# Kernel tuning notes

Measured on AMD Instinct MI355X. Metric: run time of the kernel, lower is better.

The kernel has to match this reference:

```python
import jax, jax.numpy as jnp
import numpy as np

D_MODEL, N_HEADS, D_K, D_V = 512, 8, 32, 32
LN_EPS = 1e-5


def setup_inputs() -> dict:
    key = jax.random.key(0)
    ks = jax.random.split(key, 12)
    B, L = 4, 2048
    inner = N_HEADS * D_K
    s_in = 1.0 / np.sqrt(D_MODEL)
    s_fc = 1.0 / np.sqrt(inner)
    return {
        "q": jax.random.normal(ks[0], (B, L, D_MODEL), jnp.float32),
        "k": jax.random.normal(ks[1], (B, L, D_MODEL), jnp.float32),
        "v": jax.random.normal(ks[2], (B, L, D_MODEL), jnp.float32),
        "Wq": jax.random.normal(ks[3], (inner, D_MODEL), jnp.float32) * s_in,
        "bq": jax.random.normal(ks[4], (inner,), jnp.float32) * 0.01,
        "Wk": jax.random.normal(ks[5], (inner, D_MODEL), jnp.float32) * s_in,
        "bk": jax.random.normal(ks[6], (inner,), jnp.float32) * 0.01,
        "Wv": jax.random.normal(ks[7], (N_HEADS * D_V, D_MODEL), jnp.float32) * s_in,
        "bv": jax.random.normal(ks[8], (N_HEADS * D_V,), jnp.float32) * 0.01,
        "Wfc": jax.random.normal(ks[9], (D_MODEL, N_HEADS * D_V), jnp.float32) * s_fc,
        "bfc": jax.random.normal(ks[10], (D_MODEL,), jnp.float32) * 0.01,
        "gamma": jnp.ones((D_MODEL,), jnp.float32),
        "beta": jnp.zeros((D_MODEL,), jnp.float32),
    }


def reference(q, k, v, Wq, bq, Wk, bk, Wv, bv, Wfc, bfc, gamma, beta):
    n, l, _ = q.shape
    # Projection output interpreted as (..., d_k, n_heads): head idx is fastest dim
    def split_heads(x, W, b, dh):
        p = x @ W.T + b                     # [n, l, dh*H]
        return p.reshape(n, x.shape[1], dh, N_HEADS).transpose(0, 3, 1, 2)  # [n,H,l,dh]

    qh = split_heads(q, Wq, bq, D_K)
    kh = split_heads(k, Wk, bk, D_K)
    vh = split_heads(v, Wv, bv, D_V)

    scale = 1.0 / jnp.sqrt(jnp.asarray(D_K, q.dtype))
    scores = jnp.einsum('nhqd,nhkd->nhqk', qh, kh) * scale  # [n,H,L,L]
    att = jax.nn.softmax(scores, axis=-1)
    out = jnp.einsum('nhqk,nhkd->nhqd', att, vh)             # [n,H,L,d_v]
    out = out.transpose(0, 2, 1, 3).reshape(n, l, N_HEADS * D_V)

    fc = out @ Wfc.T + bfc
    x = fc + q  # residual
    mean = jnp.mean(x, axis=-1, keepdims=True)
    var = jnp.mean(jnp.square(x - mean), axis=-1, keepdims=True)
    return gamma * (x - mean) / jnp.sqrt(var + LN_EPS) + beta
```

## Files before the change

### kernel.cpp

```cpp
#include <hip/hip_runtime.h>
#include <math.h>

constexpr int Bn = 4, Ln = 2048, DM = 512, NH = 8, DKv = 32, INNER = 256;
constexpr int TTOK = Bn * Ln;
constexpr size_t HEAD_ELEMS = (size_t)Bn * NH * Ln * DKv;


typedef short short8 __attribute__((ext_vector_type(8)));
typedef short short4v __attribute__((ext_vector_type(4)));
typedef float floatx4 __attribute__((ext_vector_type(4)));

constexpr size_t XB_OFF  = 8u * 1024 * 1024;
constexpr size_t WB_OFF  = 12536832;
constexpr size_t WFCB_OFF = WB_OFF + 3 * 131072;

constexpr float C1 = 0.25505654f;

__device__ inline short f2bf(float x) {
  unsigned u = __builtin_bit_cast(unsigned, x);
  unsigned r = (u + 0x7FFFu + ((u >> 16) & 1u)) >> 16;
  return (short)r;
}

#if __has_builtin(__builtin_amdgcn_mfma_f32_16x16x16bf16_1k)
#define MFMA16(a, b, c) __builtin_amdgcn_mfma_f32_16x16x16bf16_1k(a, b, c, 0, 0, 0)
#else
__device__ inline floatx4 mfma16_asm(short4v a, short4v b, floatx4 c) {
  asm volatile("v_mfma_f32_16x16x16_bf16 %0, %1, %2, %3\n\ts_nop 4"
               : "=v"(c) : "v"(a), "v"(b), "0"(c));
  return c;
}
#define MFMA16(a, b, c) mfma16_asm(a, b, c)
#endif

__global__ __launch_bounds__(256) void cvtw_kernel(
    const float* __restrict__ Wq, const float* __restrict__ Wk,
    const float* __restrict__ Wv, const float* __restrict__ Wfc,
    short* __restrict__ Wb, short* __restrict__ Wfcb)
{
  const int z = blockIdx.y;
  const float* src = z == 0 ? Wq : (z == 1 ? Wk : (z == 2 ? Wv : Wfc));
  short* dst = z < 3 ? Wb + (size_t)z * 131072 : Wfcb;
  const int idx = (blockIdx.x * 256 + threadIdx.x) * 4;
  float4 x = *(const float4*)&src[idx];
  *(short4v*)&dst[idx] = (short4v){f2bf(x.x), f2bf(x.y), f2bf(x.z), f2bf(x.w)};
}

__global__ __launch_bounds__(256) void proj_kernel(
    const float* __restrict__ q, const float* __restrict__ k, const float* __restrict__ v,
    const short* __restrict__ Wb,
    const float* __restrict__ bq, const float* __restrict__ bk,
    const float* __restrict__ bv,
    short* __restrict__ ws)
{
  const int mat = blockIdx.z;
  const float* X    = mat == 0 ? q  : (mat == 1 ? k  : v);
  const short* W    = Wb + (size_t)mat * 131072;
  const float* bias = mat == 0 ? bq : (mat == 1 ? bk : bv);
  short* outp = ws + (size_t)mat * HEAD_ELEMS;

  const int t0 = blockIdx.x * 64;
  const int c0 = blockIdx.y * 64;
  const int tid = threadIdx.x;
  const int col = tid & 15;
  const int quad = (tid & 63) >> 4;
  const int w = tid >> 6;

  __shared__ short Xs[64 * 136];
  __shared__ short Wsh[64 * 136];

  floatx4 acc[4];
#pragma unroll
  for (int nj = 0; nj < 4; ++nj) acc[nj] = (floatx4){0.f, 0.f, 0.f, 0.f};

  float4 xr[8];
  short8 wr[4];
  auto loadX = [&](int k0) {
#pragma unroll
    for (int j = 0; j < 8; ++j) {
      const int i = tid + j * 256, row = i >> 5, c4 = i & 31;
      xr[j] = *(const float4*)&X[(size_t)(t0 + row) * DM + k0 + c4 * 4];
    }
  };
  auto loadW = [&](int k0) {
#pragma unroll
    for (int j = 0; j < 4; ++j) {
      const int s = tid + j * 256, row = s >> 4, k8 = s & 15;
      wr[j] = *(const short8*)&W[(size_t)(c0 + row) * DM + k0 + k8 * 8];
    }
  };

  loadX(0);
  loadW(0);

  for (int kc = 0; kc < 4; ++kc) {
#pragma unroll
    for (int j = 0; j < 8; ++j) {
      const int i = tid + j * 256, row = i >> 5, c4 = i & 31;
      *(short4v*)&Xs[row * 136 + c4 * 4] =
          (short4v){f2bf(xr[j].x), f2bf(xr[j].y), f2bf(xr[j].z), f2bf(xr[j].w)};
    }
#pragma unroll
    for (int j = 0; j < 4; ++j) {
      const int s = tid + j * 256, row = s >> 4, k8 = s & 15;
      *(short8*)&Wsh[row * 136 + k8 * 8] = wr[j];
    }
    __syncthreads();
    if (kc < 3) {
      loadX((kc + 1) * 128);
      loadW((kc + 1) * 128);
    }
#pragma unroll
    for (int ks = 0; ks < 4; ++ks) {
      short8 a = *(const short8*)&Xs[(w * 16 + col) * 136 + ks * 32 + quad * 8];
#pragma unroll
      for (int nj = 0; nj < 4; ++nj) {
        short8 b = *(const short8*)&Wsh[(nj * 16 + col) * 136 + ks * 32 + quad * 8];
        acc[nj] = __builtin_amdgcn_mfma_f32_16x16x32_bf16(a, b, acc[nj], 0, 0, 0);
      }
    }
    __syncthreads();
  }

#pragma unroll
  for (int nj = 0; nj < 4; ++nj) {
#pragma unroll
    for (int r = 0; r < 4; ++r) {
      const int t = t0 + w * 16 + quad * 4 + r;
      const int n = t >> 11, ll = t & (Ln - 1);
      const int c = c0 + nj * 16 + col;
      const int d = c >> 3, h = c & 7;
      float pv = acc[nj][r] + bias[c];
      if (mat == 0) pv *= C1;
      const short val = f2bf(pv);
      if (mat < 2)
        outp[((size_t)(n * NH + h) * Ln + ll) * DKv + d] = val;
      else
        outp[((size_t)(n * NH + h) * DKv + d) * Ln + ll] = val;
    }
  }
}

__global__ __launch_bounds__(256) void attn_kernel(const short* __restrict__ ws,
                                                   short* __restrict__ O2b)
{
  const int bh = blockIdx.y;
  const int n = bh >> 3, h = bh & 7;
  const int tid = threadIdx.x;
  const int col = tid & 15;
  const int quad = (tid & 63) >> 4;
  const int w = tid >> 6;
  const int qi = blockIdx.x * 64 + w * 16 + col;

  const short* Qh = ws;
  const short* Kg = ws + HEAD_ELEMS + (size_t)bh * Ln * DKv;
  const short* Vg = ws + 2 * HEAD_ELEMS + (size_t)bh * DKv * Ln;

  __shared__ short Ks[2][64 * 32];
  __shared__ short Vs[2][64 * 32];

  const short8 aq = *(const short8*)&Qh[(size_t)bh * Ln * DKv + (size_t)qi * DKv + quad * 8];

  float lsum = 0.f;
  floatx4 o[2];
  o[0] = (floatx4){0.f, 0.f, 0.f, 0.f};
  o[1] = (floatx4){0.f, 0.f, 0.f, 0.f};

  const int vd = tid >> 3, vkb = tid & 7;
  const int voff1 = (vkb >> 1) * 512 + ((2 * vkb) & 3) * 128 + (vd & 15) * 8 + (vd >> 4) * 4;
  const int voff2 = (vkb >> 1) * 512 + ((2 * vkb + 1) & 3) * 128 + (vd & 15) * 8 + (vd >> 4) * 4;

  short8 kr = *(const short8*)(Kg + tid * 8);
  short8 vr = *(const short8*)(Vg + (size_t)vd * Ln + vkb * 8);

  for (int kt = 0; kt < 32; ++kt) {
    short* ksb = Ks[kt & 1];
    short* vsb = Vs[kt & 1];
    *(short8*)&ksb[tid * 8] = kr;
    *(short4v*)&vsb[voff1] = __builtin_shufflevector(vr, vr, 0, 1, 2, 3);
    *(short4v*)&vsb[voff2] = __builtin_shufflevector(vr, vr, 4, 5, 6, 7);
    __syncthreads();
    if (kt < 31) {
      kr = *(const short8*)(Kg + (size_t)(kt + 1) * 2048 + tid * 8);
      vr = *(const short8*)(Vg + (size_t)vd * Ln + (kt + 1) * 64 + vkb * 8);
    }

    floatx4 s[4];
    const floatx4 z4 = {0.f, 0.f, 0.f, 0.f};
#pragma unroll
    for (int ks = 0; ks < 4; ++ks) {
      short8 kf = *(const short8*)&ksb[(ks * 16 + col) * 32 + quad * 8];
      s[ks] = __builtin_amdgcn_mfma_f32_16x16x32_bf16(kf, aq, z4, 0, 0, 0);
    }

    short4v pf[4];
#pragma unroll
    for (int ks = 0; ks < 4; ++ks) {
      float p0 = __builtin_amdgcn_exp2f(s[ks][0]);
      float p1 = __builtin_amdgcn_exp2f(s[ks][1]);
      float p2 = __builtin_amdgcn_exp2f(s[ks][2]);
      float p3 = __builtin_amdgcn_exp2f(s[ks][3]);
      lsum += (p0 + p1) + (p2 + p3);
      unsigned u0 = __builtin_amdgcn_perm(__builtin_bit_cast(unsigned, p1),
                                          __builtin_bit_cast(unsigned, p0), 0x07060302u);
      unsigned u1 = __builtin_amdgcn_perm(__builtin_bit_cast(unsigned, p3),
                                          __builtin_bit_cast(unsigned, p2), 0x07060302u);
      uint2 uu = make_uint2(u0, u1);
      pf[ks] = __builtin_bit_cast(short4v, uu);
    }

#pragma unroll
    for (int ks = 0; ks < 4; ++ks) {
      short8 vv = *(const short8*)&vsb[ks * 512 + quad * 128 + col * 8];
      o[0] = MFMA16(__builtin_shufflevector(vv, vv, 0, 1, 2, 3), pf[ks], o[0]);
      o[1] = MFMA16(__builtin_shufflevector(vv, vv, 4, 5, 6, 7), pf[ks], o[1]);
    }
  }

  lsum += __shfl_xor(lsum, 16);
  lsum += __shfl_xor(lsum, 32);
  const float inv = 1.f / lsum;

  short* dst = &O2b[((size_t)n * Ln + qi) * INNER + h * DKv];
#pragma unroll
  for (int dt = 0; dt < 2; ++dt)
#pragma unroll
    for (int r = 0; r < 4; ++r)
      dst[dt * 16 + quad * 4 + r] = f2bf(o[dt][r] * inv);
}

__global__ __launch_bounds__(256) void fc_kernel(
    const short* __restrict__ O2b, const short* __restrict__ Wfcb,
    const float* __restrict__ bfc, const float* __restrict__ qin,
    short* __restrict__ Xb)
{
  const int t0 = blockIdx.x * 64;
  const int c0 = blockIdx.y * 64;
  const int tid = threadIdx.x;
  const int col = tid & 15;
  const int quad = (tid & 63) >> 4;
  const int w = tid >> 6;

  __shared__ short As[64 * 264];
  __shared__ short Bs[64 * 264];

  for (int i = tid; i < 2048; i += 256) {
    const int row = i >> 5, k8 = i & 31;
    *(short8*)&As[row * 264 + k8 * 8] =
        *(const short8*)&O2b[(size_t)(t0 + row) * INNER + k8 * 8];
    *(short8*)&Bs[row * 264 + k8 * 8] =
        *(const short8*)&Wfcb[(size_t)(c0 + row) * INNER + k8 * 8];
  }
  __syncthreads();

  floatx4 acc[4];
#pragma unroll
  for (int nj = 0; nj < 4; ++nj) acc[nj] = (floatx4){0.f, 0.f, 0.f, 0.f};

#pragma unroll
  for (int ks = 0; ks < 8; ++ks) {
    short8 a = *(const short8*)&As[(w * 16 + col) * 264 + ks * 32 + quad * 8];
#pragma unroll
    for (int nj = 0; nj < 4; ++nj) {
      short8 b = *(const short8*)&Bs[(nj * 16 + col) * 264 + ks * 32 + quad * 8];
      acc[nj] = __builtin_amdgcn_mfma_f32_16x16x32_bf16(a, b, acc[nj], 0, 0, 0);
    }
  }

#pragma unroll
  for (int nj = 0; nj < 4; ++nj) {
#pragma unroll
    for (int r = 0; r < 4; ++r) {
      const int t = t0 + w * 16 + quad * 4 + r;
      const int c = c0 + nj * 16 + col;
      Xb[(size_t)t * DM + c] = f2bf(acc[nj][r] + bfc[c] + qin[(size_t)t * DM + c]);
    }
  }
}

__global__ __launch_bounds__(256) void ln_kernel(
    const short* __restrict__ Xb, const float* __restrict__ gamma,
    const float* __restrict__ beta, float* __restrict__ outp)
{
  const int t = blockIdx.x * 4 + (threadIdx.x >> 6);
  const int lane = threadIdx.x & 63;

  short8 xs = *(const short8*)&Xb[(size_t)t * DM + lane * 8];
  float x[8];
#pragma unroll
  for (int j = 0; j < 8; ++j)
    x[j] = __builtin_bit_cast(float, ((unsigned)(unsigned short)xs[j]) << 16);

  float s1 = 0.f, s2 = 0.f;
#pragma unroll
  for (int j = 0; j < 8; ++j) { s1 += x[j]; s2 += x[j] * x[j]; }
#pragma unroll
  for (int off = 32; off >= 1; off >>= 1) {
    s1 += __shfl_xor(s1, off);
    s2 += __shfl_xor(s2, off);
  }
  const float mean = s1 * (1.f / 512.f);
  const float var = s2 * (1.f / 512.f) - mean * mean;
  const float rstd = rsqrtf(var + 1e-5f);

  float4 g0 = *(const float4*)&gamma[lane * 8];
  float4 g1 = *(const float4*)&gamma[lane * 8 + 4];
  float4 b0 = *(const float4*)&beta[lane * 8];
  float4 b1 = *(const float4*)&beta[lane * 8 + 4];

  float4 y0, y1;
  y0.x = g0.x * (x[0] - mean) * rstd + b0.x;
  y0.y = g0.y * (x[1] - mean) * rstd + b0.y;
  y0.z = g0.z * (x[2] - mean) * rstd + b0.z;
  y0.w = g0.w * (x[3] - mean) * rstd + b0.w;
  y1.x = g1.x * (x[4] - mean) * rstd + b1.x;
  y1.y = g1.y * (x[5] - mean) * rstd + b1.y;
  y1.z = g1.z * (x[6] - mean) * rstd + b1.z;
  y1.w = g1.w * (x[7] - mean) * rstd + b1.w;

  float* drow = &outp[(size_t)t * DM + lane * 8];
  *(float4*)&drow[0] = y0;
  *(float4*)&drow[4] = y1;
}

extern "C" void kernel_launch(void* const* d_in, const int* in_sizes, int n_in,
                              void* d_out, int out_size, void* d_ws, size_t ws_size,
                              hipStream_t stream) {
  const float* q     = (const float*)d_in[0];
  const float* k     = (const float*)d_in[1];
  const float* v     = (const float*)d_in[2];
  const float* Wq    = (const float*)d_in[3];
  const float* bq    = (const float*)d_in[4];
  const float* Wk    = (const float*)d_in[5];
  const float* bk    = (const float*)d_in[6];
  const float* Wv    = (const float*)d_in[7];
  const float* bv    = (const float*)d_in[8];
  const float* Wfc   = (const float*)d_in[9];
  const float* bfc   = (const float*)d_in[10];
  const float* gamma = (const float*)d_in[11];
  const float* beta  = (const float*)d_in[12];

  short* wsS  = (short*)d_ws;
  short* O2b  = wsS + 3 * HEAD_ELEMS;
  short* Xb   = wsS + XB_OFF;
  short* Wb   = wsS + WB_OFF;
  short* Wfcb = wsS + WFCB_OFF;

  cvtw_kernel<<<dim3(128, 4), 256, 0, stream>>>(Wq, Wk, Wv, Wfc, Wb, Wfcb);

  dim3 gp(TTOK / 64, INNER / 64, 3);
  proj_kernel<<<gp, 256, 0, stream>>>(q, k, v, Wb, bq, bk, bv, wsS);

  dim3 gatt(Ln / 64, Bn * NH);
  attn_kernel<<<gatt, 256, 0, stream>>>(wsS, O2b);

  dim3 gfc(TTOK / 64, DM / 64);
  fc_kernel<<<gfc, 256, 0, stream>>>(O2b, Wfcb, bfc, q, Xb);

  ln_kernel<<<TTOK / 4, 256, 0, stream>>>(Xb, gamma, beta, (float*)d_out);
}
```

Before: 194.2 us.

## Process two query tiles per warp in attention to reuse K/V shared tiles

Each warp now handles 32 query rows (two 16-row subtiles) instead of 16, so every K/V tile loaded into shared memory and every LDS fragment read feeds twice as many MFMAs. The attention grid is halved to match. The shared-memory layouts are also changed to padded row-major forms (stride 40 for K, 72 for V), which replaces the swizzled V store and is meant to avoid bank conflicts. In exchange, register pressure rises and fewer blocks are launched, which lowers parallelism.

New measurement: 187.8 us. 3.3% less time.

```diff
diff --git a/kernel.cpp b/kernel.cpp
--- a/kernel.cpp
+++ b/kernel.cpp
@@ -150,83 +150,98 @@
   const int col = tid & 15;
   const int quad = (tid & 63) >> 4;
   const int w = tid >> 6;
-  const int qi = blockIdx.x * 64 + w * 16 + col;
+  const int qb = blockIdx.x * 128 + w * 32;
 
   const short* Qh = ws;
   const short* Kg = ws + HEAD_ELEMS + (size_t)bh * Ln * DKv;
   const short* Vg = ws + 2 * HEAD_ELEMS + (size_t)bh * DKv * Ln;
 
-  __shared__ short Ks[2][64 * 32];
-  __shared__ short Vs[2][64 * 32];
-
-  const short8 aq = *(const short8*)&Qh[(size_t)bh * Ln * DKv + (size_t)qi * DKv + quad * 8];
-
-  float lsum = 0.f;
-  floatx4 o[2];
-  o[0] = (floatx4){0.f, 0.f, 0.f, 0.f};
-  o[1] = (floatx4){0.f, 0.f, 0.f, 0.f};
+  __shared__ short Ks[2][64 * 40];
+  __shared__ short Vs[2][32 * 72];
+
+  short8 aq[2];
+#pragma unroll
+  for (int si = 0; si < 2; ++si)
+    aq[si] = *(const short8*)&Qh[(size_t)bh * Ln * DKv +
+                                 (size_t)(qb + si * 16 + col) * DKv + quad * 8];
+
+  float lsum[2] = {0.f, 0.f};
+  floatx4 o[2][2];
+#pragma unroll
+  for (int si = 0; si < 2; ++si)
+#pragma unroll
+    for (int dt = 0; dt < 2; ++dt) o[si][dt] = (floatx4){0.f, 0.f, 0.f, 0.f};
 
   const int vd = tid >> 3, vkb = tid & 7;
-  const int voff1 = (vkb >> 1) * 512 + ((2 * vkb) & 3) * 128 + (vd & 15) * 8 + (vd >> 4) * 4;
-  const int voff2 = (vkb >> 1) * 512 + ((2 * vkb + 1) & 3) * 128 + (vd & 15) * 8 + (vd >> 4) * 4;
-
+  const int krow = tid >> 2, kj = tid & 3;
   short8 kr = *(const short8*)(Kg + tid * 8);
   short8 vr = *(const short8*)(Vg + (size_t)vd * Ln + vkb * 8);
 
   for (int kt = 0; kt < 32; ++kt) {
     short* ksb = Ks[kt & 1];
     short* vsb = Vs[kt & 1];
-    *(short8*)&ksb[tid * 8] = kr;
-    *(short4v*)&vsb[voff1] = __builtin_shufflevector(vr, vr, 0, 1, 2, 3);
-    *(short4v*)&vsb[voff2] = __builtin_shufflevector(vr, vr, 4, 5, 6, 7);
+    *(short8*)&ksb[krow * 40 + kj * 8] = kr;
+    *(short8*)&vsb[vd * 72 + vkb * 8] = vr;
     __syncthreads();
     if (kt < 31) {
       kr = *(const short8*)(Kg + (size_t)(kt + 1) * 2048 + tid * 8);
       vr = *(const short8*)(Vg + (size_t)vd * Ln + (kt + 1) * 64 + vkb * 8);
     }
 
-    floatx4 s[4];
+    floatx4 s[2][4];
     const floatx4 z4 = {0.f, 0.f, 0.f, 0.f};
 #pragma unroll
     for (int ks = 0; ks < 4; ++ks) {
-      short8 kf = *(const short8*)&ksb[(ks * 16 + col) * 32 + quad * 8];
-      s[ks] = __builtin_amdgcn_mfma_f32_16x16x32_bf16(kf, aq, z4, 0, 0, 0);
-    }
-
-    short4v pf[4];
+      short8 kf = *(const short8*)&ksb[(ks * 16 + col) * 40 + quad * 8];
+      s[0][ks] = __builtin_amdgcn_mfma_f32_16x16x32_bf16(kf, aq[0], z4, 0, 0, 0);
+      s[1][ks] = __builtin_amdgcn_mfma_f32_16x16x32_bf16(kf, aq[1], z4, 0, 0, 0);
+    }
+
+    short4v pf[2][4];
+#pragma unroll
+    for (int si = 0; si < 2; ++si) {
+#pragma unroll
+      for (int ks = 0; ks < 4; ++ks) {
+        float p0 = __builtin_amdgcn_exp2f(s[si][ks][0]);
+        float p1 = __builtin_amdgcn_exp2f(s[si][ks][1]);
+        float p2 = __builtin_amdgcn_exp2f(s[si][ks][2]);
+        float p3 = __builtin_amdgcn_exp2f(s[si][ks][3]);
+        lsum[si] += (p0 + p1) + (p2 + p3);
+        unsigned u0 = __builtin_amdgcn_perm(__builtin_bit_cast(unsigned, p1),
+                                            __builtin_bit_cast(unsigned, p0), 0x07060302u);
+        unsigned u1 = __builtin_amdgcn_perm(__builtin_bit_cast(unsigned, p3),
+                                            __builtin_bit_cast(unsigned, p2), 0x07060302u);
+        uint2 uu = make_uint2(u0, u1);
+        pf[si][ks] = __builtin_bit_cast(short4v, uu);
+      }
+    }
+
 #pragma unroll
     for (int ks = 0; ks < 4; ++ks) {
-      float p0 = __builtin_amdgcn_exp2f(s[ks][0]);
-      float p1 = __builtin_amdgcn_exp2f(s[ks][1]);
-      float p2 = __builtin_amdgcn_exp2f(s[ks][2]);
-      float p3 = __builtin_amdgcn_exp2f(s[ks][3]);
-      lsum += (p0 + p1) + (p2 + p3);
-      unsigned u0 = __builtin_amdgcn_perm(__builtin_bit_cast(unsigned, p1),
-                                          __builtin_bit_cast(unsigned, p0), 0x07060302u);
-      unsigned u1 = __builtin_amdgcn_perm(__builtin_bit_cast(unsigned, p3),
-                                          __builtin_bit_cast(unsigned, p2), 0x07060302u);
-      uint2 uu = make_uint2(u0, u1);
-      pf[ks] = __builtin_bit_cast(short4v, uu);
-    }
-
-#pragma unroll
-    for (int ks = 0; ks < 4; ++ks) {
-      short8 vv = *(const short8*)&vsb[ks * 512 + quad * 128 + col * 8];
-      o[0] = MFMA16(__builtin_shufflevector(vv, vv, 0, 1, 2, 3), pf[ks], o[0]);
-      o[1] = MFMA16(__builtin_shufflevector(vv, vv, 4, 5, 6, 7), pf[ks], o[1]);
-    }
-  }
-
-  lsum += __shfl_xor(lsum, 16);
-  lsum += __shfl_xor(lsum, 32);
-  const float inv = 1.f / lsum;
-
-  short* dst = &O2b[((size_t)n * Ln + qi) * INNER + h * DKv];
-#pragma unroll
-  for (int dt = 0; dt < 2; ++dt)
-#pragma unroll
-    for (int r = 0; r < 4; ++r)
-      dst[dt * 16 + quad * 4 + r] = f2bf(o[dt][r] * inv);
+      short4v va0 = *(const short4v*)&vsb[col * 72 + ks * 16 + quad * 4];
+      short4v va1 = *(const short4v*)&vsb[(16 + col) * 72 + ks * 16 + quad * 4];
+#pragma unroll
+      for (int si = 0; si < 2; ++si) {
+        o[si][0] = MFMA16(va0, pf[si][ks], o[si][0]);
+        o[si][1] = MFMA16(va1, pf[si][ks], o[si][1]);
+      }
+    }
+  }
+
+#pragma unroll
+  for (int si = 0; si < 2; ++si) {
+    float l = lsum[si];
+    l += __shfl_xor(l, 16);
+    l += __shfl_xor(l, 32);
+    const float inv = 1.f / l;
+    const int qi = qb + si * 16 + col;
+    short* dst = &O2b[((size_t)n * Ln + qi) * INNER + h * DKv];
+#pragma unroll
+    for (int dt = 0; dt < 2; ++dt)
+#pragma unroll
+      for (int r = 0; r < 4; ++r)
+        dst[dt * 16 + quad * 4 + r] = f2bf(o[si][dt][r] * inv);
+  }
 }
 
 __global__ __launch_bounds__(256) void fc_kernel(
@@ -351,7 +366,7 @@
   dim3 gp(TTOK / 64, INNER / 64, 3);
   proj_kernel<<<gp, 256, 0, stream>>>(q, k, v, Wb, bq, bk, bv, wsS);
 
-  dim3 gatt(Ln / 64, Bn * NH);
+  dim3 gatt(Ln / 128, Bn * NH);
   attn_kernel<<<gatt, 256, 0, stream>>>(wsS, O2b);
 
   dim3 gfc(TTOK / 64, DM / 64);
```

## Rewrite attention kernel with 32x32x16 MFMA tiles and MFMA row-sum

Applied to the files above, without the earlier changes.

The attention kernel now uses 32x32x16 bf16 MFMA instructions instead of 16x16 variants. Each block covers 128 queries and loads 128-key tiles into padded, swizzled shared memory. The softmax denominator is computed by an extra MFMA against a vector of ones rather than scalar adds plus cross-lane shuffles. The goal is higher matrix-core throughput, fewer LDS/sync iterations and better reuse per tile, at the cost of more accumulator registers (three floatx16 values), an extra MFMA per chunk, and half as many blocks in the grid.

New measurement: 182.7 us. -5.9%, faster.

```diff
diff --git a/kernel.cpp b/kernel.cpp
--- a/kernel.cpp
+++ b/kernel.cpp
@@ -9,6 +9,7 @@
 typedef short short8 __attribute__((ext_vector_type(8)));
 typedef short short4v __attribute__((ext_vector_type(4)));
 typedef float floatx4 __attribute__((ext_vector_type(4)));
+typedef float floatx16 __attribute__((ext_vector_type(16)));
 
 constexpr size_t XB_OFF  = 8u * 1024 * 1024;
 constexpr size_t WB_OFF  = 12536832;
@@ -21,17 +22,6 @@
   unsigned r = (u + 0x7FFFu + ((u >> 16) & 1u)) >> 16;
   return (short)r;
 }
-
-#if __has_builtin(__builtin_amdgcn_mfma_f32_16x16x16bf16_1k)
-#define MFMA16(a, b, c) __builtin_amdgcn_mfma_f32_16x16x16bf16_1k(a, b, c, 0, 0, 0)
-#else
-__device__ inline floatx4 mfma16_asm(short4v a, short4v b, floatx4 c) {
-  asm volatile("v_mfma_f32_16x16x16_bf16 %0, %1, %2, %3\n\ts_nop 4"
-               : "=v"(c) : "v"(a), "v"(b), "0"(c));
-  return c;
-}
-#define MFMA16(a, b, c) mfma16_asm(a, b, c)
-#endif
 
 __global__ __launch_bounds__(256) void cvtw_kernel(
     const float* __restrict__ Wq, const float* __restrict__ Wk,
@@ -147,86 +137,102 @@
   const int bh = blockIdx.y;
   const int n = bh >> 3, h = bh & 7;
   const int tid = threadIdx.x;
-  const int col = tid & 15;
-  const int quad = (tid & 63) >> 4;
+  const int lane = tid & 63;
+  const int col = lane & 31;
+  const int hf = lane >> 5;
   const int w = tid >> 6;
-  const int qi = blockIdx.x * 64 + w * 16 + col;
+  const int qi = blockIdx.x * 128 + w * 32 + col;
 
   const short* Qh = ws;
   const short* Kg = ws + HEAD_ELEMS + (size_t)bh * Ln * DKv;
   const short* Vg = ws + 2 * HEAD_ELEMS + (size_t)bh * DKv * Ln;
 
-  __shared__ short Ks[2][64 * 32];
-  __shared__ short Vs[2][64 * 32];
-
-  const short8 aq = *(const short8*)&Qh[(size_t)bh * Ln * DKv + (size_t)qi * DKv + quad * 8];
-
-  float lsum = 0.f;
-  floatx4 o[2];
-  o[0] = (floatx4){0.f, 0.f, 0.f, 0.f};
-  o[1] = (floatx4){0.f, 0.f, 0.f, 0.f};
-
+  __shared__ short Ks[2][128 * 40];
+  __shared__ short Vs[2][32 * 136];
+
+  short8 aq[2];
+#pragma unroll
+  for (int c = 0; c < 2; ++c)
+    aq[c] = *(const short8*)&Qh[(size_t)bh * Ln * DKv + (size_t)qi * DKv + c * 16 + hf * 8];
+
+  short8 ones;
+#pragma unroll
+  for (int j = 0; j < 8; ++j) ones[j] = (short)0x3F80;
+
+  floatx16 o, ol;
+#pragma unroll
+  for (int i = 0; i < 16; ++i) { o[i] = 0.f; ol[i] = 0.f; }
+
+  const int kg = tid >> 1, khalf = tid & 1;
+  const int krow = (kg & ~12) | ((kg & 4) << 1) | ((kg & 8) >> 1);
+  const int kst = krow * 40 + khalf * 16;
   const int vd = tid >> 3, vkb = tid & 7;
-  const int voff1 = (vkb >> 1) * 512 + ((2 * vkb) & 3) * 128 + (vd & 15) * 8 + (vd >> 4) * 4;
-  const int voff2 = (vkb >> 1) * 512 + ((2 * vkb + 1) & 3) * 128 + (vd & 15) * 8 + (vd >> 4) * 4;
-
-  short8 kr = *(const short8*)(Kg + tid * 8);
-  short8 vr = *(const short8*)(Vg + (size_t)vd * Ln + vkb * 8);
-
-  for (int kt = 0; kt < 32; ++kt) {
+  const int vst = vd * 136 + vkb * 16;
+
+  short8 kr0 = *(const short8*)(Kg + kg * 32 + khalf * 16);
+  short8 kr1 = *(const short8*)(Kg + kg * 32 + khalf * 16 + 8);
+  short8 vr0 = *(const short8*)(Vg + (size_t)vd * Ln + vkb * 16);
+  short8 vr1 = *(const short8*)(Vg + (size_t)vd * Ln + vkb * 16 + 8);
+
+  for (int kt = 0; kt < 16; ++kt) {
     short* ksb = Ks[kt & 1];
     short* vsb = Vs[kt & 1];
-    *(short8*)&ksb[tid * 8] = kr;
-    *(short4v*)&vsb[voff1] = __builtin_shufflevector(vr, vr, 0, 1, 2, 3);
-    *(short4v*)&vsb[voff2] = __builtin_shufflevector(vr, vr, 4, 5, 6, 7);
+    *(short8*)&ksb[kst] = kr0;
+    *(short8*)&ksb[kst + 8] = kr1;
+    *(short8*)&vsb[vst] = vr0;
+    *(short8*)&vsb[vst + 8] = vr1;
     __syncthreads();
-    if (kt < 31) {
-      kr = *(const short8*)(Kg + (size_t)(kt + 1) * 2048 + tid * 8);
-      vr = *(const short8*)(Vg + (size_t)vd * Ln + (kt + 1) * 64 + vkb * 8);
-    }
-
-    floatx4 s[4];
-    const floatx4 z4 = {0.f, 0.f, 0.f, 0.f};
-#pragma unroll
-    for (int ks = 0; ks < 4; ++ks) {
-      short8 kf = *(const short8*)&ksb[(ks * 16 + col) * 32 + quad * 8];
-      s[ks] = __builtin_amdgcn_mfma_f32_16x16x32_bf16(kf, aq, z4, 0, 0, 0);
-    }
-
-    short4v pf[4];
-#pragma unroll
-    for (int ks = 0; ks < 4; ++ks) {
-      float p0 = __builtin_amdgcn_exp2f(s[ks][0]);
-      float p1 = __builtin_amdgcn_exp2f(s[ks][1]);
-      float p2 = __builtin_amdgcn_exp2f(s[ks][2]);
-      float p3 = __builtin_amdgcn_exp2f(s[ks][3]);
-      lsum += (p0 + p1) + (p2 + p3);
-      unsigned u0 = __builtin_amdgcn_perm(__builtin_bit_cast(unsigned, p1),
-                                          __builtin_bit_cast(unsigned, p0), 0x07060302u);
-      unsigned u1 = __builtin_amdgcn_perm(__builtin_bit_cast(unsigned, p3),
-                                          __builtin_bit_cast(unsigned, p2), 0x07060302u);
-      uint2 uu = make_uint2(u0, u1);
-      pf[ks] = __builtin_bit_cast(short4v, uu);
-    }
-
-#pragma unroll
-    for (int ks = 0; ks < 4; ++ks) {
-      short8 vv = *(const short8*)&vsb[ks * 512 + quad * 128 + col * 8];
-      o[0] = MFMA16(__builtin_shufflevector(vv, vv, 0, 1, 2, 3), pf[ks], o[0]);
-      o[1] = MFMA16(__builtin_shufflevector(vv, vv, 4, 5, 6, 7), pf[ks], o[1]);
-    }
-  }
-
-  lsum += __shfl_xor(lsum, 16);
-  lsum += __shfl_xor(lsum, 32);
-  const float inv = 1.f / lsum;
-
+    if (kt < 15) {
+      kr0 = *(const short8*)(Kg + (size_t)(kt + 1) * 4096 + kg * 32 + khalf * 16);
+      kr1 = *(const short8*)(Kg + (size_t)(kt + 1) * 4096 + kg * 32 + khalf * 16 + 8);
+      vr0 = *(const short8*)(Vg + (size_t)vd * Ln + (kt + 1) * 128 + vkb * 16);
+      vr1 = *(const short8*)(Vg + (size_t)vd * Ln + (kt + 1) * 128 + vkb * 16 + 8);
+    }
+
+#pragma unroll
+    for (int cc = 0; cc < 4; ++cc) {
+      floatx16 st;
+#pragma unroll
+      for (int i = 0; i < 16; ++i) st[i] = 0.f;
+      short8 kf0 = *(const short8*)&ksb[(cc * 32 + col) * 40 + hf * 8];
+      short8 kf1 = *(const short8*)&ksb[(cc * 32 + col) * 40 + 16 + hf * 8];
+      st = __builtin_amdgcn_mfma_f32_32x32x16_bf16(kf0, aq[0], st, 0, 0, 0);
+      st = __builtin_amdgcn_mfma_f32_32x32x16_bf16(kf1, aq[1], st, 0, 0, 0);
+
+      float p[16];
+#pragma unroll
+      for (int i = 0; i < 16; ++i) p[i] = __builtin_amdgcn_exp2f(st[i]);
+      short8 pf[2];
+#pragma unroll
+      for (int half = 0; half < 2; ++half) {
+        unsigned u[4];
+#pragma unroll
+        for (int j = 0; j < 4; ++j)
+          u[j] = __builtin_amdgcn_perm(
+              __builtin_bit_cast(unsigned, p[half * 8 + 2 * j + 1]),
+              __builtin_bit_cast(unsigned, p[half * 8 + 2 * j]), 0x07060302u);
+        uint4 uu = make_uint4(u[0], u[1], u[2], u[3]);
+        pf[half] = __builtin_bit_cast(short8, uu);
+      }
+
+      ol = __builtin_amdgcn_mfma_f32_32x32x16_bf16(ones, pf[0], ol, 0, 0, 0);
+      ol = __builtin_amdgcn_mfma_f32_32x32x16_bf16(ones, pf[1], ol, 0, 0, 0);
+
+      short8 va0 = *(const short8*)&vsb[col * 136 + cc * 32 + hf * 8];
+      short8 va1 = *(const short8*)&vsb[col * 136 + cc * 32 + 16 + hf * 8];
+      o = __builtin_amdgcn_mfma_f32_32x32x16_bf16(va0, pf[0], o, 0, 0, 0);
+      o = __builtin_amdgcn_mfma_f32_32x32x16_bf16(va1, pf[1], o, 0, 0, 0);
+    }
+  }
+
+  const float inv = 1.f / ol[0];
   short* dst = &O2b[((size_t)n * Ln + qi) * INNER + h * DKv];
 #pragma unroll
-  for (int dt = 0; dt < 2; ++dt)
-#pragma unroll
-    for (int r = 0; r < 4; ++r)
-      dst[dt * 16 + quad * 4 + r] = f2bf(o[dt][r] * inv);
+  for (int g4 = 0; g4 < 4; ++g4) {
+    short4v pk = (short4v){f2bf(o[g4 * 4 + 0] * inv), f2bf(o[g4 * 4 + 1] * inv),
+                           f2bf(o[g4 * 4 + 2] * inv), f2bf(o[g4 * 4 + 3] * inv)};
+    *(short4v*)&dst[8 * g4 + 4 * hf] = pk;
+  }
 }
 
 __global__ __launch_bounds__(256) void fc_kernel(
@@ -351,7 +357,7 @@
   dim3 gp(TTOK / 64, INNER / 64, 3);
   proj_kernel<<<gp, 256, 0, stream>>>(q, k, v, Wb, bq, bk, bv, wsS);
 
-  dim3 gatt(Ln / 64, Bn * NH);
+  dim3 gatt(Ln / 128, Bn * NH);
   attn_kernel<<<gatt, 256, 0, stream>>>(wsS, O2b);
 
   dim3 gfc(TTOK / 64, DM / 64);
```
